# Kernel optimization log

Hardware: AMD Instinct MI355X
Metric: run time of the kernel (lower is better)

## Reference

```python
import jax, jax.numpy as jnp
import numpy as np


def setup_inputs() -> dict:
    key = jax.random.key(0)
    kX, kA, kB, kC = jax.random.split(key, 4)
    Bsz, L, H, P, S = 2, 4096, 16, 64, 64
    X = jax.random.normal(kX, (Bsz, L, H, P), jnp.float32)
    # log-space negative decay per head (docstring: 'scalar decay per head (log space, negative)')
    A = -0.1 * jax.random.uniform(kA, (Bsz, L, H), jnp.float32)
    Bm = jax.random.normal(kB, (Bsz, L, H, S), jnp.float32) / np.sqrt(S).astype(np.float32)
    Cm = jax.random.normal(kC, (Bsz, L, H, S), jnp.float32) / np.sqrt(S).astype(np.float32)
    return {"X": X, "A": A, "B": Bm, "C": Cm, "chunk_size": 64}


def _ssd_forward(X, A, B, C, chunk_size):
    batch, seqlen, H, P = X.shape
    S = B.shape[-1]
    cs = chunk_size
    orig_seqlen = seqlen
    pad = (-seqlen) % cs
    if pad:
        X = jnp.pad(X, ((0, 0), (0, pad), (0, 0), (0, 0)))
        A = jnp.pad(A, ((0, 0), (0, pad), (0, 0)))
        B = jnp.pad(B, ((0, 0), (0, pad), (0, 0), (0, 0)))
        C = jnp.pad(C, ((0, 0), (0, pad), (0, 0), (0, 0)))
        seqlen = seqlen + pad
    n = seqlen // cs
    # reshape to chunks and move heads forward: [b, h, n, c, ...]
    Xc = X.reshape(batch, n, cs, H, P).transpose(0, 3, 1, 2, 4)
    Ac = A.reshape(batch, n, cs, H).transpose(0, 3, 1, 2)          # [b,h,n,c]
    Bc = B.reshape(batch, n, cs, H, S).transpose(0, 3, 1, 2, 4)
    Cc = C.reshape(batch, n, cs, H, S).transpose(0, 3, 1, 2, 4)
    Acs = jnp.cumsum(Ac, axis=-1)                                   # [b,h,n,c]
    # causal decay matrix L: exp(A_i - A_j) for i>=j; masked entries get -inf
    # then clamp(-inf, -100, 100) -> -100, exp(-100) ~ 3.7e-44 (faithful to torch order)
    diff = Acs[..., :, None] - Acs[..., None, :]                    # [b,h,n,c,c]
    causal = jnp.arange(cs)[:, None] >= jnp.arange(cs)[None, :]
    log_diff = jnp.clip(jnp.where(causal, diff, -jnp.inf), -100.0, 100.0)
    Lmat = jnp.nan_to_num(jnp.exp(log_diff), nan=0.0, posinf=1.0, neginf=0.0)
    # intra-chunk (attention-like) term
    CB = jnp.einsum('bhnis,bhnjs->bhnij', Cc, Bc)
    Y_intra = jnp.einsum('bhnij,bhnjp->bhnip', Lmat * CB, Xc)
    # inter-chunk state recurrence
    decay_chunk = jnp.exp(jnp.sum(Ac, axis=-1))                     # [b,h,n]
    decay_to_end = jnp.exp(Acs[..., -1:] - Acs)                     # [b,h,n,c]
    h_final = jnp.einsum('bhnc,bhncs,bhncp->bhnsp', decay_to_end, Bc, Xc)
    def step(carry, xs):
        d, hf = xs
        new_carry = d[..., None, None] * carry + hf
        return new_carry, carry  # h_inter[c] is state BEFORE chunk c
    d_scan = jnp.moveaxis(decay_chunk, 2, 0)                        # [n,b,h]
    h_scan = jnp.moveaxis(h_final, 2, 0)                            # [n,b,h,s,p]
    init = jnp.zeros((batch, H, S, P), X.dtype)
    _, h_inter = jax.lax.scan(step, init, (d_scan, h_scan))
    h_inter = jnp.moveaxis(h_inter, 0, 2)                           # [b,h,n,s,p]
    decay_from_start = jnp.exp(Acs)
    Y_inter = jnp.einsum('bhnis,bhnsp,bhni->bhnip', Cc, h_inter, decay_from_start)
    Y = (Y_intra + Y_inter).transpose(0, 2, 3, 1, 4).reshape(batch, seqlen, H, P)
    return Y[:, :orig_seqlen]


def reference(X, A, B, C, chunk_size):
    return _ssd_forward(X, A, B, C, chunk_size)
```

## Files before the change

### kernel.cpp

```cpp
#include <hip/hip_runtime.h>


#define BSZ 2
#define LSEQ 4096
#define NH 16
#define NC 64
#define SCAN_G 8
#define HWS_ELEMS ((size_t)BSZ * NH * NC * 64 * 64)

typedef float f32x4 __attribute__((ext_vector_type(4)));
typedef __bf16 bf16x8 __attribute__((ext_vector_type(8)));

union FragU { uint4 u; bf16x8 b; };

__device__ __forceinline__ unsigned short f2b(float x) {
    union { float f; unsigned u; } c; c.f = x;
    unsigned r = c.u + 0x7fffu + ((c.u >> 16) & 1u);
    return (unsigned short)(r >> 16);
}
__device__ __forceinline__ float b2f(unsigned short v) {
    union { unsigned u; float f; } c; c.u = ((unsigned)v) << 16;
    return c.f;
}

__device__ __forceinline__ int rm_e(int row, int k) { return row * 64 + (k ^ ((row & 7) << 3)); }
__device__ __forceinline__ int tr_e(int row, int k) { return row * 64 + (k ^ (((row >> 1) & 7) << 3)); }

__device__ __forceinline__ bf16x8 frag_rm(const unsigned short* buf, int tile, int kk, int l) {
    FragU f; f.u = *(const uint4*)&buf[rm_e(tile * 16 + (l & 15), kk * 32 + ((l >> 4) << 3))];
    return f.b;
}
__device__ __forceinline__ bf16x8 frag_tr(const unsigned short* buf, int tile, int kk, int l) {
    FragU f; f.u = *(const uint4*)&buf[tr_e(tile * 16 + (l & 15), kk * 32 + ((l >> 4) << 3))];
    return f.b;
}

__global__ __launch_bounds__(256) void ssd_hfinal(
    const float* __restrict__ Xg, const float* __restrict__ Ag,
    const float* __restrict__ Bg, unsigned short* __restrict__ hws,
    float* __restrict__ dws)
{
    __shared__ __align__(16) unsigned short sBt[64 * 64];
    __shared__ __align__(16) unsigned short sXt[64 * 64];
    __shared__ float sDte[64];

    const int tid = threadIdx.x;
    const int l = tid & 63;
    const int w = tid >> 6;
    const int n = blockIdx.x & (NC - 1);
    const int h = (blockIdx.x >> 6) & (NH - 1);
    const int b = blockIdx.x >> 10;
    const int row0 = b * LSEQ + n * 64;

    float4 xv[4], bv[4];
    const int p0 = (tid & 15) * 4;
    #pragma unroll
    for (int it = 0; it < 4; ++it) {
        const int c = (tid >> 4) + it * 16;
        const unsigned g = ((unsigned)(row0 + c) * NH + h) * 64 + p0;
        xv[it] = *(const float4*)&Xg[g];
        bv[it] = *(const float4*)&Bg[g];
    }
    if (tid < 64) {
        float a = Ag[(unsigned)(row0 + tid) * NH + h];
        #pragma unroll
        for (int off = 1; off < 64; off <<= 1) {
            float v = __shfl_up(a, off, 64);
            if (tid >= off) a += v;
        }
        const float a63 = __shfl(a, 63, 64);
        sDte[tid] = __expf(a63 - a);
        if (tid == 63) dws[(b * NH + h) * NC + n] = __expf(a63);
    }
    __syncthreads();

    #pragma unroll
    for (int it = 0; it < 4; ++it) {
        const int c = (tid >> 4) + it * 16;
        const float dte = sDte[c];
        sBt[tr_e(p0 + 0, c)] = f2b(bv[it].x);
        sBt[tr_e(p0 + 1, c)] = f2b(bv[it].y);
        sBt[tr_e(p0 + 2, c)] = f2b(bv[it].z);
        sBt[tr_e(p0 + 3, c)] = f2b(bv[it].w);
        sXt[tr_e(p0 + 0, c)] = f2b(xv[it].x * dte);
        sXt[tr_e(p0 + 1, c)] = f2b(xv[it].y * dte);
        sXt[tr_e(p0 + 2, c)] = f2b(xv[it].z * dte);
        sXt[tr_e(p0 + 3, c)] = f2b(xv[it].w * dte);
    }
    __syncthreads();

    const f32x4 zero = {0.f, 0.f, 0.f, 0.f};
    f32x4 acc[4] = {zero, zero, zero, zero};
    #pragma unroll
    for (int kk = 0; kk < 2; ++kk) {
        const bf16x8 aB = frag_tr(sBt, w, kk, l);
        #pragma unroll
        for (int tp = 0; tp < 4; ++tp)
            acc[tp] = __builtin_amdgcn_mfma_f32_16x16x32_bf16(aB, frag_tr(sXt, tp, kk, l), acc[tp], 0, 0, 0);
    }

    const unsigned hb = ((unsigned)((b * NH + h) * NC + n)) * 4096u;
    const int sbase = w * 16 + ((l >> 4) << 2);
    #pragma unroll
    for (int tp = 0; tp < 4; ++tp) {
        const int p = tp * 16 + (l & 15);
        ushort4 o;
        o.x = f2b(acc[tp][0]); o.y = f2b(acc[tp][1]);
        o.z = f2b(acc[tp][2]); o.w = f2b(acc[tp][3]);
        *(ushort4*)&hws[hb + (unsigned)p * 64 + sbase] = o;
    }
}

__global__ __launch_bounds__(256) void ssd_scan(unsigned short* __restrict__ hws,
                                                const float* __restrict__ dws)
{
    __shared__ float sD[NC];
    const int tid = threadIdx.x;
    const int bh = blockIdx.x / SCAN_G;
    const int g = blockIdx.x % SCAN_G;
    if (tid < NC) sD[tid] = dws[bh * NC + tid];
    __syncthreads();

    unsigned* hw32 = (unsigned*)hws;
    const unsigned base = (unsigned)bh * NC * 2048u + g * 256u + tid;
    float cx = 0.f, cy = 0.f;
    unsigned cur = hw32[base];
    #pragma unroll 4
    for (int c = 0; c < NC; ++c) {
        unsigned nxt = 0;
        if (c < NC - 1) nxt = hw32[base + (c + 1) * 2048u];
        const float hx = b2f((unsigned short)(cur & 0xffffu));
        const float hy = b2f((unsigned short)(cur >> 16));
        hw32[base + c * 2048u] = (unsigned)f2b(cx) | ((unsigned)f2b(cy) << 16);
        const float d = sD[c];
        cx = d * cx + hx;
        cy = d * cy + hy;
        cur = nxt;
    }
}

__global__ __launch_bounds__(256) void ssd_y(
    const float* __restrict__ Xg, const float* __restrict__ Ag,
    const float* __restrict__ Bg, const float* __restrict__ Cg,
    const unsigned short* __restrict__ hws, float* __restrict__ Yg)
{
    __shared__ __align__(16) unsigned short sBM[64 * 64];
    __shared__ __align__(16) unsigned short sC[64 * 64];
    __shared__ __align__(16) unsigned short sXt[64 * 64];
    __shared__ __align__(16) unsigned short sH[64 * 64];
    __shared__ float sE[64], sR[64];

    const int tid = threadIdx.x;
    const int l = tid & 63;
    const int w = tid >> 6;
    const int n = blockIdx.x & (NC - 1);
    const int h = (blockIdx.x >> 6) & (NH - 1);
    const int b = blockIdx.x >> 10;
    const int row0 = b * LSEQ + n * 64;
    const unsigned hb = ((unsigned)((b * NH + h) * NC + n)) * 4096u;

    if (tid < 64) {
        float a = Ag[(unsigned)(row0 + tid) * NH + h];
        #pragma unroll
        for (int off = 1; off < 64; off <<= 1) {
            float v = __shfl_up(a, off, 64);
            if (tid >= off) a += v;
        }
        sE[tid] = __expf(a);
        sR[tid] = __expf(-a);
    }
    {
        const int p0 = (tid & 15) * 4;
        #pragma unroll
        for (int it = 0; it < 4; ++it) {
            const int c = (tid >> 4) + it * 16;
            const unsigned g = ((unsigned)(row0 + c) * NH + h) * 64 + p0;
            const float4 xv = *(const float4*)&Xg[g];
            const float4 bv = *(const float4*)&Bg[g];
            const float4 cv = *(const float4*)&Cg[g];
            ushort4 bw; bw.x = f2b(bv.x); bw.y = f2b(bv.y); bw.z = f2b(bv.z); bw.w = f2b(bv.w);
            ushort4 cw; cw.x = f2b(cv.x); cw.y = f2b(cv.y); cw.z = f2b(cv.z); cw.w = f2b(cv.w);
            *(ushort4*)&sBM[rm_e(c, p0)] = bw;
            *(ushort4*)&sC[rm_e(c, p0)] = cw;
            sXt[tr_e(p0 + 0, c)] = f2b(xv.x);
            sXt[tr_e(p0 + 1, c)] = f2b(xv.y);
            sXt[tr_e(p0 + 2, c)] = f2b(xv.z);
            sXt[tr_e(p0 + 3, c)] = f2b(xv.w);
        }
    }
    {
        const int pr = tid >> 2;
        const int s0 = (tid & 3) * 16;
        const uint4 h0 = *(const uint4*)&hws[hb + (unsigned)pr * 64 + s0];
        const uint4 h1 = *(const uint4*)&hws[hb + (unsigned)pr * 64 + s0 + 8];
        *(uint4*)&sH[rm_e(pr, s0)] = h0;
        *(uint4*)&sH[rm_e(pr, s0 + 8)] = h1;
    }
    __syncthreads();

    const f32x4 zero = {0.f, 0.f, 0.f, 0.f};
    const int il = (l >> 4) << 2;

    f32x4 accCB[4] = {zero, zero, zero, zero};
    #pragma unroll
    for (int kk = 0; kk < 2; ++kk) {
        const bf16x8 aC = frag_rm(sC, w, kk, l);
        #pragma unroll
        for (int tj = 0; tj < 4; ++tj)
            accCB[tj] = __builtin_amdgcn_mfma_f32_16x16x32_bf16(aC, frag_rm(sBM, tj, kk, l), accCB[tj], 0, 0, 0);
    }
    __syncthreads();

    #pragma unroll
    for (int tj = 0; tj < 4; ++tj) {
        #pragma unroll
        for (int r = 0; r < 4; ++r) {
            const int i = w * 16 + il + r;
            const int j = tj * 16 + (l & 15);
            const float v = (i >= j) ? sE[i] * sR[j] * accCB[tj][r] : 0.f;
            sBM[i * 64 + (j ^ ((i & 7) << 3))] = f2b(v);
        }
    }
    __syncthreads();

    f32x4 accY[4] = {zero, zero, zero, zero};
    f32x4 accI[4] = {zero, zero, zero, zero};
    #pragma unroll
    for (int kk = 0; kk < 2; ++kk) {
        const bf16x8 aX = frag_tr(sXt, w, kk, l);
        const bf16x8 aH = frag_rm(sH, w, kk, l);
        #pragma unroll
        for (int ti = 0; ti < 4; ++ti) {
            accY[ti] = __builtin_amdgcn_mfma_f32_16x16x32_bf16(aX, frag_rm(sBM, ti, kk, l), accY[ti], 0, 0, 0);
            accI[ti] = __builtin_amdgcn_mfma_f32_16x16x32_bf16(aH, frag_rm(sC, ti, kk, l), accI[ti], 0, 0, 0);
        }
    }

    const int pbase = w * 16 + il;
    #pragma unroll
    for (int ti = 0; ti < 4; ++ti) {
        const int i = ti * 16 + (l & 15);
        const float dfs = sE[i];
        float4 o;
        o.x = accY[ti][0] + dfs * accI[ti][0];
        o.y = accY[ti][1] + dfs * accI[ti][1];
        o.z = accY[ti][2] + dfs * accI[ti][2];
        o.w = accY[ti][3] + dfs * accI[ti][3];
        *(float4*)&Yg[((unsigned)(row0 + i) * NH + h) * 64 + pbase] = o;
    }
}

extern "C" void kernel_launch(void* const* d_in, const int* in_sizes, int n_in,
                              void* d_out, int out_size, void* d_ws, size_t ws_size,
                              hipStream_t stream) {
    const float* X = (const float*)d_in[0];
    const float* A = (const float*)d_in[1];
    const float* Bm = (const float*)d_in[2];
    const float* Cm = (const float*)d_in[3];
    float* Y = (float*)d_out;
    unsigned short* hws = (unsigned short*)d_ws;
    float* dws = (float*)(hws + HWS_ELEMS);

    ssd_hfinal<<<BSZ * NH * NC, 256, 0, stream>>>(X, A, Bm, hws, dws);
    ssd_scan<<<BSZ * NH * SCAN_G, 256, 0, stream>>>(hws, dws);
    ssd_y<<<BSZ * NH * NC, 256, 0, stream>>>(X, A, Bm, Cm, hws, Y);
}
```

Before: 57.33 us.

## Precompute masked CB and decay-scaled C tiles in first kernel, simplify Y kernel

The first kernel now also loads C and computes the masked, decay-weighted C·Bᵀ matrix and the exp(Acs)-scaled C tile. It writes both to workspace as bf16 alongside a swizzled chunk state. The Y kernel then drops its LDS staging, the cumsum and the CB matmul. It loads X fragments straight from global memory and reads the M and Cs fragments from workspace. This shortens the dependent phases of the last kernel, but adds workspace writes and reads, moves C reads into the first kernel, and does strided scalar X loads in the Y kernel.

After: 66.83 us. 16.6% more time.

```diff
diff --git a/kernel.cpp b/kernel.cpp
--- a/kernel.cpp
+++ b/kernel.cpp
@@ -5,8 +5,10 @@
 #define LSEQ 4096
 #define NH 16
 #define NC 64
+#define NCH (BSZ * NH * NC)
 #define SCAN_G 8
-#define HWS_ELEMS ((size_t)BSZ * NH * NC * 64 * 64)
+#define CHW 4096
+#define TILE_USHORTS ((size_t)NCH * CHW)
 
 typedef float f32x4 __attribute__((ext_vector_type(4)));
 typedef __bf16 bf16x8 __attribute__((ext_vector_type(8)));
@@ -35,14 +37,17 @@
     return f.b;
 }
 
-__global__ __launch_bounds__(256) void ssd_hfinal(
+__global__ __launch_bounds__(256) void ssd_k1(
     const float* __restrict__ Xg, const float* __restrict__ Ag,
-    const float* __restrict__ Bg, unsigned short* __restrict__ hws,
-    float* __restrict__ dws)
+    const float* __restrict__ Bg, const float* __restrict__ Cg,
+    unsigned short* __restrict__ hws, unsigned short* __restrict__ Mws,
+    unsigned short* __restrict__ Csws, float* __restrict__ dws)
 {
+    __shared__ __align__(16) unsigned short sBrm[64 * 64];
+    __shared__ __align__(16) unsigned short sCrm[64 * 64];
     __shared__ __align__(16) unsigned short sBt[64 * 64];
     __shared__ __align__(16) unsigned short sXt[64 * 64];
-    __shared__ float sDte[64];
+    __shared__ float sE[64], sR[64], sDte[64];
 
     const int tid = threadIdx.x;
     const int l = tid & 63;
@@ -51,8 +56,9 @@
     const int h = (blockIdx.x >> 6) & (NH - 1);
     const int b = blockIdx.x >> 10;
     const int row0 = b * LSEQ + n * 64;
-
-    float4 xv[4], bv[4];
+    const unsigned chb = (unsigned)blockIdx.x * CHW;
+
+    float4 xv[4], bv[4], cv[4];
     const int p0 = (tid & 15) * 4;
     #pragma unroll
     for (int it = 0; it < 4; ++it) {
@@ -60,6 +66,7 @@
         const unsigned g = ((unsigned)(row0 + c) * NH + h) * 64 + p0;
         xv[it] = *(const float4*)&Xg[g];
         bv[it] = *(const float4*)&Bg[g];
+        cv[it] = *(const float4*)&Cg[g];
     }
     if (tid < 64) {
         float a = Ag[(unsigned)(row0 + tid) * NH + h];
@@ -69,8 +76,10 @@
             if (tid >= off) a += v;
         }
         const float a63 = __shfl(a, 63, 64);
+        sE[tid] = __expf(a);
+        sR[tid] = __expf(-a);
         sDte[tid] = __expf(a63 - a);
-        if (tid == 63) dws[(b * NH + h) * NC + n] = __expf(a63);
+        if (tid == 63) dws[blockIdx.x] = __expf(a63);
     }
     __syncthreads();
 
@@ -78,36 +87,63 @@
     for (int it = 0; it < 4; ++it) {
         const int c = (tid >> 4) + it * 16;
         const float dte = sDte[c];
-        sBt[tr_e(p0 + 0, c)] = f2b(bv[it].x);
-        sBt[tr_e(p0 + 1, c)] = f2b(bv[it].y);
-        sBt[tr_e(p0 + 2, c)] = f2b(bv[it].z);
-        sBt[tr_e(p0 + 3, c)] = f2b(bv[it].w);
+        const float Ec = sE[c];
+        ushort4 bw; bw.x = f2b(bv[it].x); bw.y = f2b(bv[it].y); bw.z = f2b(bv[it].z); bw.w = f2b(bv[it].w);
+        ushort4 cw; cw.x = f2b(cv[it].x); cw.y = f2b(cv[it].y); cw.z = f2b(cv[it].z); cw.w = f2b(cv[it].w);
+        *(ushort4*)&sBrm[rm_e(c, p0)] = bw;
+        *(ushort4*)&sCrm[rm_e(c, p0)] = cw;
+        sBt[tr_e(p0 + 0, c)] = bw.x;
+        sBt[tr_e(p0 + 1, c)] = bw.y;
+        sBt[tr_e(p0 + 2, c)] = bw.z;
+        sBt[tr_e(p0 + 3, c)] = bw.w;
         sXt[tr_e(p0 + 0, c)] = f2b(xv[it].x * dte);
         sXt[tr_e(p0 + 1, c)] = f2b(xv[it].y * dte);
         sXt[tr_e(p0 + 2, c)] = f2b(xv[it].z * dte);
         sXt[tr_e(p0 + 3, c)] = f2b(xv[it].w * dte);
+        ushort4 sw; sw.x = f2b(cv[it].x * Ec); sw.y = f2b(cv[it].y * Ec);
+        sw.z = f2b(cv[it].z * Ec); sw.w = f2b(cv[it].w * Ec);
+        *(ushort4*)&Csws[chb + rm_e(c, p0)] = sw;
     }
     __syncthreads();
 
     const f32x4 zero = {0.f, 0.f, 0.f, 0.f};
-    f32x4 acc[4] = {zero, zero, zero, zero};
+    f32x4 accT[4] = {zero, zero, zero, zero};
+    f32x4 accH[4] = {zero, zero, zero, zero};
     #pragma unroll
     for (int kk = 0; kk < 2; ++kk) {
-        const bf16x8 aB = frag_tr(sBt, w, kk, l);
-        #pragma unroll
-        for (int tp = 0; tp < 4; ++tp)
-            acc[tp] = __builtin_amdgcn_mfma_f32_16x16x32_bf16(aB, frag_tr(sXt, tp, kk, l), acc[tp], 0, 0, 0);
-    }
-
-    const unsigned hb = ((unsigned)((b * NH + h) * NC + n)) * 4096u;
-    const int sbase = w * 16 + ((l >> 4) << 2);
+        const bf16x8 aB = frag_rm(sBrm, w, kk, l);
+        const bf16x8 aBt = frag_tr(sBt, w, kk, l);
+        #pragma unroll
+        for (int t = 0; t < 4; ++t) {
+            accT[t] = __builtin_amdgcn_mfma_f32_16x16x32_bf16(aB, frag_rm(sCrm, t, kk, l), accT[t], 0, 0, 0);
+            accH[t] = __builtin_amdgcn_mfma_f32_16x16x32_bf16(aBt, frag_tr(sXt, t, kk, l), accH[t], 0, 0, 0);
+        }
+    }
+
+    const int il = (l >> 4) << 2;
+    const int j0 = w * 16 + il;
+    float Rj[4];
+    #pragma unroll
+    for (int r = 0; r < 4; ++r) Rj[r] = sR[j0 + r];
+    #pragma unroll
+    for (int ti = 0; ti < 4; ++ti) {
+        const int i = ti * 16 + (l & 15);
+        const float Ei = sE[i];
+        ushort4 m;
+        m.x = (i >= j0 + 0) ? f2b(Ei * Rj[0] * accT[ti][0]) : (unsigned short)0;
+        m.y = (i >= j0 + 1) ? f2b(Ei * Rj[1] * accT[ti][1]) : (unsigned short)0;
+        m.z = (i >= j0 + 2) ? f2b(Ei * Rj[2] * accT[ti][2]) : (unsigned short)0;
+        m.w = (i >= j0 + 3) ? f2b(Ei * Rj[3] * accT[ti][3]) : (unsigned short)0;
+        *(ushort4*)&Mws[chb + rm_e(i, j0)] = m;
+    }
+    const int s0 = w * 16 + il;
     #pragma unroll
     for (int tp = 0; tp < 4; ++tp) {
         const int p = tp * 16 + (l & 15);
         ushort4 o;
-        o.x = f2b(acc[tp][0]); o.y = f2b(acc[tp][1]);
-        o.z = f2b(acc[tp][2]); o.w = f2b(acc[tp][3]);
-        *(ushort4*)&hws[hb + (unsigned)p * 64 + sbase] = o;
+        o.x = f2b(accH[tp][0]); o.y = f2b(accH[tp][1]);
+        o.z = f2b(accH[tp][2]); o.w = f2b(accH[tp][3]);
+        *(ushort4*)&hws[chb + rm_e(p, s0)] = o;
     }
 }
 
@@ -139,17 +175,11 @@
     }
 }
 
-__global__ __launch_bounds__(256) void ssd_y(
-    const float* __restrict__ Xg, const float* __restrict__ Ag,
-    const float* __restrict__ Bg, const float* __restrict__ Cg,
-    const unsigned short* __restrict__ hws, float* __restrict__ Yg)
+__global__ __launch_bounds__(256) void ssd_k3(
+    const float* __restrict__ Xg, const unsigned short* __restrict__ Mws,
+    const unsigned short* __restrict__ Csws, const unsigned short* __restrict__ hws,
+    float* __restrict__ Yg)
 {
-    __shared__ __align__(16) unsigned short sBM[64 * 64];
-    __shared__ __align__(16) unsigned short sC[64 * 64];
-    __shared__ __align__(16) unsigned short sXt[64 * 64];
-    __shared__ __align__(16) unsigned short sH[64 * 64];
-    __shared__ float sE[64], sR[64];
-
     const int tid = threadIdx.x;
     const int l = tid & 63;
     const int w = tid >> 6;
@@ -157,95 +187,48 @@
     const int h = (blockIdx.x >> 6) & (NH - 1);
     const int b = blockIdx.x >> 10;
     const int row0 = b * LSEQ + n * 64;
-    const unsigned hb = ((unsigned)((b * NH + h) * NC + n)) * 4096u;
-
-    if (tid < 64) {
-        float a = Ag[(unsigned)(row0 + tid) * NH + h];
-        #pragma unroll
-        for (int off = 1; off < 64; off <<= 1) {
-            float v = __shfl_up(a, off, 64);
-            if (tid >= off) a += v;
-        }
-        sE[tid] = __expf(a);
-        sR[tid] = __expf(-a);
-    }
-    {
-        const int p0 = (tid & 15) * 4;
-        #pragma unroll
-        for (int it = 0; it < 4; ++it) {
-            const int c = (tid >> 4) + it * 16;
-            const unsigned g = ((unsigned)(row0 + c) * NH + h) * 64 + p0;
-            const float4 xv = *(const float4*)&Xg[g];
-            const float4 bv = *(const float4*)&Bg[g];
-            const float4 cv = *(const float4*)&Cg[g];
-            ushort4 bw; bw.x = f2b(bv.x); bw.y = f2b(bv.y); bw.z = f2b(bv.z); bw.w = f2b(bv.w);
-            ushort4 cw; cw.x = f2b(cv.x); cw.y = f2b(cv.y); cw.z = f2b(cv.z); cw.w = f2b(cv.w);
-            *(ushort4*)&sBM[rm_e(c, p0)] = bw;
-            *(ushort4*)&sC[rm_e(c, p0)] = cw;
-            sXt[tr_e(p0 + 0, c)] = f2b(xv.x);
-            sXt[tr_e(p0 + 1, c)] = f2b(xv.y);
-            sXt[tr_e(p0 + 2, c)] = f2b(xv.z);
-            sXt[tr_e(p0 + 3, c)] = f2b(xv.w);
-        }
-    }
-    {
-        const int pr = tid >> 2;
-        const int s0 = (tid & 3) * 16;
-        const uint4 h0 = *(const uint4*)&hws[hb + (unsigned)pr * 64 + s0];
-        const uint4 h1 = *(const uint4*)&hws[hb + (unsigned)pr * 64 + s0 + 8];
-        *(uint4*)&sH[rm_e(pr, s0)] = h0;
-        *(uint4*)&sH[rm_e(pr, s0 + 8)] = h1;
-    }
-    __syncthreads();
+    const unsigned chb = (unsigned)blockIdx.x * CHW;
+
+    const int p = w * 16 + (l & 15);
+    bf16x8 aX[2], aH[2];
+    #pragma unroll
+    for (int kk = 0; kk < 2; ++kk) {
+        const int c0 = kk * 32 + ((l >> 4) << 3);
+        bf16x8 x;
+        #pragma unroll
+        for (int e = 0; e < 8; ++e)
+            x[e] = (__bf16)Xg[((unsigned)(row0 + c0 + e) * NH + h) * 64 + p];
+        aX[kk] = x;
+        FragU f; f.u = *(const uint4*)&hws[chb + rm_e(p, c0)];
+        aH[kk] = f.b;
+    }
 
     const f32x4 zero = {0.f, 0.f, 0.f, 0.f};
-    const int il = (l >> 4) << 2;
-
-    f32x4 accCB[4] = {zero, zero, zero, zero};
-    #pragma unroll
-    for (int kk = 0; kk < 2; ++kk) {
-        const bf16x8 aC = frag_rm(sC, w, kk, l);
-        #pragma unroll
-        for (int tj = 0; tj < 4; ++tj)
-            accCB[tj] = __builtin_amdgcn_mfma_f32_16x16x32_bf16(aC, frag_rm(sBM, tj, kk, l), accCB[tj], 0, 0, 0);
-    }
-    __syncthreads();
-
-    #pragma unroll
-    for (int tj = 0; tj < 4; ++tj) {
-        #pragma unroll
-        for (int r = 0; r < 4; ++r) {
-            const int i = w * 16 + il + r;
-            const int j = tj * 16 + (l & 15);
-            const float v = (i >= j) ? sE[i] * sR[j] * accCB[tj][r] : 0.f;
-            sBM[i * 64 + (j ^ ((i & 7) << 3))] = f2b(v);
-        }
-    }
-    __syncthreads();
-
     f32x4 accY[4] = {zero, zero, zero, zero};
     f32x4 accI[4] = {zero, zero, zero, zero};
     #pragma unroll
     for (int kk = 0; kk < 2; ++kk) {
-        const bf16x8 aX = frag_tr(sXt, w, kk, l);
-        const bf16x8 aH = frag_rm(sH, w, kk, l);
         #pragma unroll
         for (int ti = 0; ti < 4; ++ti) {
-            accY[ti] = __builtin_amdgcn_mfma_f32_16x16x32_bf16(aX, frag_rm(sBM, ti, kk, l), accY[ti], 0, 0, 0);
-            accI[ti] = __builtin_amdgcn_mfma_f32_16x16x32_bf16(aH, frag_rm(sC, ti, kk, l), accI[ti], 0, 0, 0);
+            const int ke = kk * 32 + ((l >> 4) << 3);
+            const int ic = ti * 16 + (l & 15);
+            FragU mf; mf.u = *(const uint4*)&Mws[chb + rm_e(ic, ke)];
+            FragU cf; cf.u = *(const uint4*)&Csws[chb + rm_e(ic, ke)];
+            accY[ti] = __builtin_amdgcn_mfma_f32_16x16x32_bf16(aX[kk], mf.b, accY[ti], 0, 0, 0);
+            accI[ti] = __builtin_amdgcn_mfma_f32_16x16x32_bf16(aH[kk], cf.b, accI[ti], 0, 0, 0);
         }
     }
 
+    const int il = (l >> 4) << 2;
     const int pbase = w * 16 + il;
     #pragma unroll
     for (int ti = 0; ti < 4; ++ti) {
         const int i = ti * 16 + (l & 15);
-        const float dfs = sE[i];
         float4 o;
-        o.x = accY[ti][0] + dfs * accI[ti][0];
-        o.y = accY[ti][1] + dfs * accI[ti][1];
-        o.z = accY[ti][2] + dfs * accI[ti][2];
-        o.w = accY[ti][3] + dfs * accI[ti][3];
+        o.x = accY[ti][0] + accI[ti][0];
+        o.y = accY[ti][1] + accI[ti][1];
+        o.z = accY[ti][2] + accI[ti][2];
+        o.w = accY[ti][3] + accI[ti][3];
         *(float4*)&Yg[((unsigned)(row0 + i) * NH + h) * 64 + pbase] = o;
     }
 }
@@ -259,9 +242,11 @@
     const float* Cm = (const float*)d_in[3];
     float* Y = (float*)d_out;
     unsigned short* hws = (unsigned short*)d_ws;
-    float* dws = (float*)(hws + HWS_ELEMS);
-
-    ssd_hfinal<<<BSZ * NH * NC, 256, 0, stream>>>(X, A, Bm, hws, dws);
+    unsigned short* Mws = hws + TILE_USHORTS;
+    unsigned short* Csws = Mws + TILE_USHORTS;
+    float* dws = (float*)(Csws + TILE_USHORTS);
+
+    ssd_k1<<<NCH, 256, 0, stream>>>(X, A, Bm, Cm, hws, Mws, Csws, dws);
     ssd_scan<<<BSZ * NH * SCAN_G, 256, 0, stream>>>(hws, dws);
-    ssd_y<<<BSZ * NH * NC, 256, 0, stream>>>(X, A, Bm, Cm, hws, Y);
-}
+    ssd_k3<<<NCH, 256, 0, stream>>>(X, Mws, Csws, hws, Y);
+}
```

## Restructure SSD output kernel: reorient MFMAs, drop barriers, prefetch loads, deepen scan

Applied to the files above, without the earlier changes.

The Y kernel now issues all global loads of X, B, C and the state tile into registers up front, before the cumsum shuffle. It reorients the matmuls so each wave owns 16 output rows, reuses the C fragments held in registers for both the CB and inter-chunk products, and writes the masked decay matrix over the C buffer, so two barriers go away. The scan kernel keeps four loads in flight instead of one to hide global latency in the serial recurrence. The final Y stores become scalar, less coalesced writes, and the wave-private overwrite of sC relies on each wave touching only its own rows.

Result: slower. 70.78 us (+23.5%).

```diff
diff --git a/kernel.cpp b/kernel.cpp
--- a/kernel.cpp
+++ b/kernel.cpp
@@ -5,13 +5,15 @@
 #define LSEQ 4096
 #define NH 16
 #define NC 64
+#define NCH (BSZ * NH * NC)
 #define SCAN_G 8
-#define HWS_ELEMS ((size_t)BSZ * NH * NC * 64 * 64)
+#define CHW 4096
+#define TILE_USHORTS ((size_t)NCH * CHW)
 
 typedef float f32x4 __attribute__((ext_vector_type(4)));
 typedef __bf16 bf16x8 __attribute__((ext_vector_type(8)));
 
-union FragU { uint4 u; bf16x8 b; };
+union FragU { uint4 u; bf16x8 b; unsigned short s[8]; };
 
 __device__ __forceinline__ unsigned short f2b(float x) {
     union { float f; unsigned u; } c; c.f = x;
@@ -51,9 +53,10 @@
     const int h = (blockIdx.x >> 6) & (NH - 1);
     const int b = blockIdx.x >> 10;
     const int row0 = b * LSEQ + n * 64;
+    const unsigned chb = (unsigned)blockIdx.x * CHW;
+    const int p0 = (tid & 15) * 4;
 
     float4 xv[4], bv[4];
-    const int p0 = (tid & 15) * 4;
     #pragma unroll
     for (int it = 0; it < 4; ++it) {
         const int c = (tid >> 4) + it * 16;
@@ -70,7 +73,7 @@
         }
         const float a63 = __shfl(a, 63, 64);
         sDte[tid] = __expf(a63 - a);
-        if (tid == 63) dws[(b * NH + h) * NC + n] = __expf(a63);
+        if (tid == 63) dws[blockIdx.x] = __expf(a63);
     }
     __syncthreads();
 
@@ -99,7 +102,6 @@
             acc[tp] = __builtin_amdgcn_mfma_f32_16x16x32_bf16(aB, frag_tr(sXt, tp, kk, l), acc[tp], 0, 0, 0);
     }
 
-    const unsigned hb = ((unsigned)((b * NH + h) * NC + n)) * 4096u;
     const int sbase = w * 16 + ((l >> 4) << 2);
     #pragma unroll
     for (int tp = 0; tp < 4; ++tp) {
@@ -107,7 +109,7 @@
         ushort4 o;
         o.x = f2b(acc[tp][0]); o.y = f2b(acc[tp][1]);
         o.z = f2b(acc[tp][2]); o.w = f2b(acc[tp][3]);
-        *(ushort4*)&hws[hb + (unsigned)p * 64 + sbase] = o;
+        *(ushort4*)&hws[chb + (unsigned)p * 64 + sbase] = o;
     }
 }
 
@@ -123,19 +125,20 @@
 
     unsigned* hw32 = (unsigned*)hws;
     const unsigned base = (unsigned)bh * NC * 2048u + g * 256u + tid;
+
+    unsigned buf[4];
+    #pragma unroll
+    for (int jj = 0; jj < 4; ++jj) buf[jj] = hw32[base + jj * 2048u];
+
     float cx = 0.f, cy = 0.f;
-    unsigned cur = hw32[base];
     #pragma unroll 4
     for (int c = 0; c < NC; ++c) {
-        unsigned nxt = 0;
-        if (c < NC - 1) nxt = hw32[base + (c + 1) * 2048u];
-        const float hx = b2f((unsigned short)(cur & 0xffffu));
-        const float hy = b2f((unsigned short)(cur >> 16));
-        hw32[base + c * 2048u] = (unsigned)f2b(cx) | ((unsigned)f2b(cy) << 16);
+        const unsigned cur = buf[c & 3];
+        if (c + 4 < NC) buf[c & 3] = hw32[base + (unsigned)(c + 4) * 2048u];
+        hw32[base + (unsigned)c * 2048u] = (unsigned)f2b(cx) | ((unsigned)f2b(cy) << 16);
         const float d = sD[c];
-        cx = d * cx + hx;
-        cy = d * cy + hy;
-        cur = nxt;
+        cx = d * cx + b2f((unsigned short)(cur & 0xffffu));
+        cy = d * cy + b2f((unsigned short)(cur >> 16));
     }
 }
 
@@ -144,10 +147,10 @@
     const float* __restrict__ Bg, const float* __restrict__ Cg,
     const unsigned short* __restrict__ hws, float* __restrict__ Yg)
 {
-    __shared__ __align__(16) unsigned short sBM[64 * 64];
+    __shared__ __align__(16) unsigned short sB[64 * 64];
     __shared__ __align__(16) unsigned short sC[64 * 64];
     __shared__ __align__(16) unsigned short sXt[64 * 64];
-    __shared__ __align__(16) unsigned short sH[64 * 64];
+    __shared__ __align__(16) unsigned short sHt[64 * 64];
     __shared__ float sE[64], sR[64];
 
     const int tid = threadIdx.x;
@@ -157,7 +160,23 @@
     const int h = (blockIdx.x >> 6) & (NH - 1);
     const int b = blockIdx.x >> 10;
     const int row0 = b * LSEQ + n * 64;
-    const unsigned hb = ((unsigned)((b * NH + h) * NC + n)) * 4096u;
+    const unsigned chb = (unsigned)blockIdx.x * CHW;
+    const int i15 = l & 15;
+    const int p0 = (tid & 15) * 4;
+
+    float4 xv[4], bv[4], cv[4];
+    #pragma unroll
+    for (int it = 0; it < 4; ++it) {
+        const int c = (tid >> 4) + it * 16;
+        const unsigned g = ((unsigned)(row0 + c) * NH + h) * 64 + p0;
+        xv[it] = *(const float4*)&Xg[g];
+        bv[it] = *(const float4*)&Bg[g];
+        cv[it] = *(const float4*)&Cg[g];
+    }
+    const int pr = tid >> 2;
+    const int sh0 = (tid & 3) << 4;
+    const uint4 h0 = *(const uint4*)&hws[chb + (unsigned)pr * 64 + sh0];
+    const uint4 h1 = *(const uint4*)&hws[chb + (unsigned)pr * 64 + sh0 + 8];
 
     if (tid < 64) {
         float a = Ag[(unsigned)(row0 + tid) * NH + h];
@@ -169,84 +188,72 @@
         sE[tid] = __expf(a);
         sR[tid] = __expf(-a);
     }
-    {
-        const int p0 = (tid & 15) * 4;
-        #pragma unroll
-        for (int it = 0; it < 4; ++it) {
-            const int c = (tid >> 4) + it * 16;
-            const unsigned g = ((unsigned)(row0 + c) * NH + h) * 64 + p0;
-            const float4 xv = *(const float4*)&Xg[g];
-            const float4 bv = *(const float4*)&Bg[g];
-            const float4 cv = *(const float4*)&Cg[g];
-            ushort4 bw; bw.x = f2b(bv.x); bw.y = f2b(bv.y); bw.z = f2b(bv.z); bw.w = f2b(bv.w);
-            ushort4 cw; cw.x = f2b(cv.x); cw.y = f2b(cv.y); cw.z = f2b(cv.z); cw.w = f2b(cv.w);
-            *(ushort4*)&sBM[rm_e(c, p0)] = bw;
-            *(ushort4*)&sC[rm_e(c, p0)] = cw;
-            sXt[tr_e(p0 + 0, c)] = f2b(xv.x);
-            sXt[tr_e(p0 + 1, c)] = f2b(xv.y);
-            sXt[tr_e(p0 + 2, c)] = f2b(xv.z);
-            sXt[tr_e(p0 + 3, c)] = f2b(xv.w);
-        }
-    }
-    {
-        const int pr = tid >> 2;
-        const int s0 = (tid & 3) * 16;
-        const uint4 h0 = *(const uint4*)&hws[hb + (unsigned)pr * 64 + s0];
-        const uint4 h1 = *(const uint4*)&hws[hb + (unsigned)pr * 64 + s0 + 8];
-        *(uint4*)&sH[rm_e(pr, s0)] = h0;
-        *(uint4*)&sH[rm_e(pr, s0 + 8)] = h1;
-    }
-    __syncthreads();
+
+    #pragma unroll
+    for (int it = 0; it < 4; ++it) {
+        const int c = (tid >> 4) + it * 16;
+        ushort4 bw; bw.x = f2b(bv[it].x); bw.y = f2b(bv[it].y); bw.z = f2b(bv[it].z); bw.w = f2b(bv[it].w);
+        ushort4 cw; cw.x = f2b(cv[it].x); cw.y = f2b(cv[it].y); cw.z = f2b(cv[it].z); cw.w = f2b(cv[it].w);
+        *(ushort4*)&sB[rm_e(c, p0)] = bw;
+        *(ushort4*)&sC[rm_e(c, p0)] = cw;
+        sXt[tr_e(p0 + 0, c)] = f2b(xv[it].x);
+        sXt[tr_e(p0 + 1, c)] = f2b(xv[it].y);
+        sXt[tr_e(p0 + 2, c)] = f2b(xv[it].z);
+        sXt[tr_e(p0 + 3, c)] = f2b(xv[it].w);
+    }
+    *(uint4*)&sHt[rm_e(pr, sh0)] = h0;
+    *(uint4*)&sHt[rm_e(pr, sh0 + 8)] = h1;
+    __syncthreads();
+
+    bf16x8 aC[2];
+    #pragma unroll
+    for (int kk = 0; kk < 2; ++kk) aC[kk] = frag_rm(sC, w, kk, l);
 
     const f32x4 zero = {0.f, 0.f, 0.f, 0.f};
+    f32x4 accT[4] = {zero, zero, zero, zero};
+    #pragma unroll
+    for (int kk = 0; kk < 2; ++kk) {
+        #pragma unroll
+        for (int tj = 0; tj < 4; ++tj)
+            accT[tj] = __builtin_amdgcn_mfma_f32_16x16x32_bf16(aC[kk], frag_rm(sB, tj, kk, l), accT[tj], 0, 0, 0);
+    }
+
     const int il = (l >> 4) << 2;
-
-    f32x4 accCB[4] = {zero, zero, zero, zero};
-    #pragma unroll
-    for (int kk = 0; kk < 2; ++kk) {
-        const bf16x8 aC = frag_rm(sC, w, kk, l);
-        #pragma unroll
-        for (int tj = 0; tj < 4; ++tj)
-            accCB[tj] = __builtin_amdgcn_mfma_f32_16x16x32_bf16(aC, frag_rm(sBM, tj, kk, l), accCB[tj], 0, 0, 0);
-    }
-    __syncthreads();
-
+    float Ei[4];
+    #pragma unroll
+    for (int r = 0; r < 4; ++r) Ei[r] = sE[w * 16 + il + r];
     #pragma unroll
     for (int tj = 0; tj < 4; ++tj) {
+        const int j = tj * 16 + i15;
+        const float Rj = sR[j];
         #pragma unroll
         for (int r = 0; r < 4; ++r) {
             const int i = w * 16 + il + r;
-            const int j = tj * 16 + (l & 15);
-            const float v = (i >= j) ? sE[i] * sR[j] * accCB[tj][r] : 0.f;
-            sBM[i * 64 + (j ^ ((i & 7) << 3))] = f2b(v);
-        }
-    }
-    __syncthreads();
+            const float v = (i >= j) ? Ei[r] * Rj * accT[tj][r] : 0.f;
+            sC[i * 64 + (j ^ ((i & 7) << 3))] = f2b(v);
+        }
+    }
 
     f32x4 accY[4] = {zero, zero, zero, zero};
     f32x4 accI[4] = {zero, zero, zero, zero};
     #pragma unroll
     for (int kk = 0; kk < 2; ++kk) {
-        const bf16x8 aX = frag_tr(sXt, w, kk, l);
-        const bf16x8 aH = frag_rm(sH, w, kk, l);
-        #pragma unroll
-        for (int ti = 0; ti < 4; ++ti) {
-            accY[ti] = __builtin_amdgcn_mfma_f32_16x16x32_bf16(aX, frag_rm(sBM, ti, kk, l), accY[ti], 0, 0, 0);
-            accI[ti] = __builtin_amdgcn_mfma_f32_16x16x32_bf16(aH, frag_rm(sC, ti, kk, l), accI[ti], 0, 0, 0);
-        }
-    }
-
-    const int pbase = w * 16 + il;
-    #pragma unroll
-    for (int ti = 0; ti < 4; ++ti) {
-        const int i = ti * 16 + (l & 15);
-        const float dfs = sE[i];
-        float4 o;
-        o.x = accY[ti][0] + dfs * accI[ti][0];
-        o.y = accY[ti][1] + dfs * accI[ti][1];
-        o.z = accY[ti][2] + dfs * accI[ti][2];
-        o.w = accY[ti][3] + dfs * accI[ti][3];
-        *(float4*)&Yg[((unsigned)(row0 + i) * NH + h) * 64 + pbase] = o;
+        const bf16x8 aM = frag_rm(sC, w, kk, l);
+        #pragma unroll
+        for (int tp = 0; tp < 4; ++tp) {
+            accY[tp] = __builtin_amdgcn_mfma_f32_16x16x32_bf16(aM, frag_tr(sXt, tp, kk, l), accY[tp], 0, 0, 0);
+            accI[tp] = __builtin_amdgcn_mfma_f32_16x16x32_bf16(aC[kk], frag_rm(sHt, tp, kk, l), accI[tp], 0, 0, 0);
+        }
+    }
+
+    #pragma unroll
+    for (int tp = 0; tp < 4; ++tp) {
+        const int p = tp * 16 + i15;
+        #pragma unroll
+        for (int r = 0; r < 4; ++r) {
+            const int i = w * 16 + il + r;
+            Yg[((unsigned)(row0 + i) * NH + h) * 64 + p] = accY[tp][r] + Ei[r] * accI[tp][r];
+        }
     }
 }
 
@@ -259,9 +266,9 @@
     const float* Cm = (const float*)d_in[3];
     float* Y = (float*)d_out;
     unsigned short* hws = (unsigned short*)d_ws;
-    float* dws = (float*)(hws + HWS_ELEMS);
-
-    ssd_hfinal<<<BSZ * NH * NC, 256, 0, stream>>>(X, A, Bm, hws, dws);
+    float* dws = (float*)(hws + TILE_USHORTS);
+
+    ssd_hfinal<<<NCH, 256, 0, stream>>>(X, A, Bm, hws, dws);
     ssd_scan<<<BSZ * NH * SCAN_G, 256, 0, stream>>>(hws, dws);
-    ssd_y<<<BSZ * NH * NC, 256, 0, stream>>>(X, A, Bm, Cm, hws, Y);
-}
+    ssd_y<<<NCH, 256, 0, stream>>>(X, A, Bm, Cm, hws, Y);
+}
```
